# Kernel tuning notes

Hardware: AMD Instinct MI355X
Metric: run time of the kernel (lower is better)

The kernel has to match this reference:

```python
import jax, jax.numpy as jnp
import numpy as np

N, E, D, R = 50000, 625000, 128, 200
BN_EPS = 1e-5


def setup_inputs() -> dict:
    key = jax.random.key(0)
    ks = jax.random.split(key, 16)
    x = jax.random.normal(ks[0], (N, D), dtype=jnp.float32)
    r_feats = jax.random.normal(ks[1], (R, D), dtype=jnp.float32)
    src = jax.random.randint(ks[2], (E,), 0, N, dtype=jnp.int32)
    dst = jax.random.randint(ks[3], (E,), 0, N, dtype=jnp.int32)
    etype = jax.random.randint(ks[4], (E,), 0, R, dtype=jnp.int32)
    norm = jax.random.uniform(ks[5], (E, 1), dtype=jnp.float32)
    out_edges_mask = jax.random.randint(ks[6], (E,), 0, 2) == 1
    in_edges_mask = jnp.logical_not(out_edges_mask)  # masks partition edges
    s = 1.0 / np.sqrt(D)
    def lin(k):
        kw, kb = jax.random.split(k)
        return (jax.random.uniform(kw, (D, D), jnp.float32, -s, s),
                jax.random.uniform(kb, (D,), jnp.float32, -s, s))
    W_O_w, W_O_b = lin(ks[7])
    W_I_w, W_I_b = lin(ks[8])
    W_S_w, W_S_b = lin(ks[9])
    W_R_w, W_R_b = lin(ks[10])
    loop_rel = jax.random.normal(ks[11], (1, D), dtype=jnp.float32) * s  # xavier-ish
    bn_gamma = jnp.ones((D,), jnp.float32)
    bn_beta = jnp.zeros((D,), jnp.float32)
    return {"x": x, "r_feats": r_feats, "src": src, "dst": dst, "etype": etype,
            "norm": norm, "in_edges_mask": in_edges_mask, "out_edges_mask": out_edges_mask,
            "W_O_w": W_O_w, "W_O_b": W_O_b, "W_I_w": W_I_w, "W_I_b": W_I_b,
            "W_S_w": W_S_w, "W_S_b": W_S_b, "W_R_w": W_R_w, "W_R_b": W_R_b,
            "loop_rel": loop_rel, "bn_gamma": bn_gamma, "bn_beta": bn_beta}


def reference(x, r_feats, src, dst, etype, norm, in_edges_mask, out_edges_mask,
              W_O_w, W_O_b, W_I_w, W_I_b, W_S_w, W_S_b, W_R_w, W_R_b,
              loop_rel, bn_gamma, bn_beta):
    # r_feats with self-loop relation appended: [R+1, D]
    r_ext = jnp.concatenate([r_feats, loop_rel], axis=0)
    # per-edge relation feature scaled by norm: [E, D]
    e_h = r_ext[etype] * norm
    # compose (sub): u_sub_e -> src feature minus edge feature
    comp_h = x[src] - e_h
    # per-direction linear projections, selected by the edge partition masks
    h_O = comp_h @ W_O_w.T + W_O_b
    h_I = comp_h @ W_I_w.T + W_I_b
    new_comp_h = jnp.where(out_edges_mask[:, None], h_O, h_I)
    # scatter-sum messages to destination nodes: [N, D]
    agg = jax.ops.segment_sum(new_comp_h, dst, num_segments=x.shape[0])
    # self-loop branch (sub with loop relation)
    comp_h_s = x - r_ext[-1]
    n_out = (comp_h_s @ W_S_w.T + W_S_b + agg) * (1.0 / 3.0)  # dropout in eval mode
    # BatchNorm1d (training-mode batch stats, biased variance)
    mean = jnp.mean(n_out, axis=0)
    var = jnp.mean((n_out - mean) ** 2, axis=0)
    n_out = (n_out - mean) * jax.lax.rsqrt(var + BN_EPS) * bn_gamma + bn_beta
    n_out = jnp.tanh(n_out)
    r_out = r_ext @ W_R_w.T + W_R_b
    return n_out, r_out[:-1]
```

## Files before the change

### kernel.cpp

```cpp
#include <hip/hip_runtime.h>
#include <cstddef>

#define N_NODES 50000
#define N_EDGES 625000
#define DIM     128
#define R_REL   200
#define BN_EPS  1e-5f
#define SLOTS   64
#define ND4     ((N_NODES * DIM) / 4)
#define R4      ((R_REL * DIM) / 4)

typedef __bf16 bf16x8 __attribute__((ext_vector_type(8)));
typedef float  f32x4  __attribute__((ext_vector_type(4)));

__device__ __forceinline__ float bfu2f(unsigned int hi16) {
    return __uint_as_float(hi16);
}
__device__ __forceinline__ unsigned int f2bfr(float f) {
    unsigned int u = __float_as_uint(f);
    return (u + 0x7fffu + ((u >> 16) & 1u)) >> 16;
}

__global__ __launch_bounds__(256) void init_kernel(
    const float* __restrict__ x, ushort* __restrict__ xb,
    const float* __restrict__ rf, ushort* __restrict__ rb,
    int* __restrict__ cnt, float* __restrict__ colsum, float* __restrict__ colsq,
    const unsigned char* __restrict__ in_m, const unsigned char* __restrict__ out_m,
    int* __restrict__ flag) {
    int gid = blockIdx.x * 256 + threadIdx.x;
    int total = gridDim.x * 256;
    for (int i = gid; i < ND4; i += total) {
        float4 v = ((const float4*)x)[i];
        ushort4 o;
        o.x = (ushort)f2bfr(v.x); o.y = (ushort)f2bfr(v.y);
        o.z = (ushort)f2bfr(v.z); o.w = (ushort)f2bfr(v.w);
        ((ushort4*)xb)[i] = o;
    }
    if (gid < R4) {
        float4 v = ((const float4*)rf)[gid];
        ushort4 o;
        o.x = (ushort)f2bfr(v.x); o.y = (ushort)f2bfr(v.y);
        o.z = (ushort)f2bfr(v.z); o.w = (ushort)f2bfr(v.w);
        ((ushort4*)rb)[gid] = o;
    }
    for (int i = gid; i < N_NODES; i += total) cnt[i] = 0;
    if (gid < DIM) { colsum[gid] = 0.f; colsq[gid] = 0.f; }
    if (blockIdx.x == 0) {
        int ok = (((int)in_m[threadIdx.x] + (int)out_m[threadIdx.x]) == 1) ? 1 : 0;
        __shared__ int sred[4];
        unsigned long long b = __ballot(ok);
        if ((threadIdx.x & 63) == 0) sred[threadIdx.x >> 6] = (b == ~0ULL) ? 1 : 0;
        __syncthreads();
        if (threadIdx.x == 0) *flag = sred[0] & sred[1] & sred[2] & sred[3];
    }
}

__global__ __launch_bounds__(384) void prep_weights_kernel(
    const float* __restrict__ WO, const float* __restrict__ WI,
    const float* __restrict__ WS, const float* __restrict__ loop,
    const float* __restrict__ bS, const float* __restrict__ bO,
    const float* __restrict__ bI, ushort* __restrict__ Wb,
    float* __restrict__ bias0, float* __restrict__ bO3, float* __restrict__ bI3) {
    int f = blockIdx.x;
    int k = threadIdx.x;
    const float third = 1.0f / 3.0f;
    float w;
    if (k < 128)      w = WS[f * DIM + k];
    else if (k < 256) w = WO[f * DIM + (k - 128)];
    else              w = WI[f * DIM + (k - 256)];
    Wb[f * 384 + k] = (ushort)f2bfr(w * third);
    __shared__ float red[128];
    if (k < 128) red[k] = loop[k] * WS[f * DIM + k];
    __syncthreads();
    for (int off = 64; off; off >>= 1) {
        if (k < off) red[k] += red[k + off];
        __syncthreads();
    }
    if (k == 0)   bias0[f] = (bS[f] - red[0]) * third;
    if (k == 64)  bO3[f] = bO[f] * third;
    if (k == 128) bI3[f] = bI[f] * third;
}

__global__ __launch_bounds__(128) void rout_kernel(const float* __restrict__ rf,
                                                   const float* __restrict__ WR,
                                                   const float* __restrict__ bR,
                                                   float* __restrict__ out) {
    int r = blockIdx.x;
    int f = threadIdx.x;
    __shared__ float row[DIM];
    row[f] = rf[r * DIM + f];
    __syncthreads();
    float acc = bR[f];
    for (int k = 0; k < DIM; ++k) acc += row[k] * WR[f * DIM + k];
    out[r * DIM + f] = acc;
}

__global__ __launch_bounds__(256) void slot_fill_kernel(
    const int* __restrict__ dst, const int* __restrict__ src,
    const int* __restrict__ et, const float* __restrict__ norm,
    const void* __restrict__ omask, const int* __restrict__ flag,
    int* __restrict__ cnt, uint2* __restrict__ erec) {
    int e = blockIdx.x * 256 + threadIdx.x;
    if (e >= N_EDGES) return;
    int fl = *flag;
    bool m = fl ? (((const unsigned char*)omask)[e] != 0)
                : (((const int*)omask)[e] != 0);
    int d = dst[e];
    int k = atomicAdd(&cnt[d], 1);
    if (k < SLOTS) {
        unsigned w0 = (unsigned)src[e] | ((unsigned)et[e] << 16) | (m ? 0x80000000u : 0u);
        erec[(size_t)d * SLOTS + k] = make_uint2(w0, (unsigned)__float_as_int(norm[e]));
    }
}

#define AGG_CALC(EX, EY, XW, RW)                                   \
    {                                                              \
        float nm = __uint_as_float(EY);                            \
        float fm = (float)((EX) >> 31);                            \
        float x0 = bfu2f((XW) << 16), x1 = bfu2f((XW) & 0xffff0000u); \
        float r0 = bfu2f((RW) << 16), r1 = bfu2f((RW) & 0xffff0000u); \
        float v0 = __builtin_fmaf(-nm, r0, x0);                    \
        float v1 = __builtin_fmaf(-nm, r1, x1);                    \
        aT0 += v0; aT1 += v1;                                      \
        aO0 = __builtin_fmaf(fm, v0, aO0);                         \
        aO1 = __builtin_fmaf(fm, v1, aO1);                         \
        cOf += fm;                                                 \
    }

__global__ __launch_bounds__(256, 8) void aggregate_kernel(
    const unsigned int* __restrict__ xb,
    const unsigned int* __restrict__ rb,
    const uint2* __restrict__ erec,
    const int* __restrict__ cnt,
    unsigned int* __restrict__ S_Ob, unsigned int* __restrict__ S_Ib,
    float* __restrict__ cntO, float* __restrict__ cntI) {
    int wv = threadIdx.x >> 6;
    unsigned lane = threadIdx.x & 63;
    int n = blockIdx.x * 4 + wv;
    if (n >= N_NODES) return;
    int deg = cnt[n];
    deg = deg < SLOTS ? deg : SLOTS;
    int beg = n * SLOTS, end = beg + deg;

    float aT0 = 0.f, aT1 = 0.f, aO0 = 0.f, aO1 = 0.f, cOf = 0.f;

    int j = beg;
    for (; j + 7 < end; j += 8) {
        uint2 e0 = erec[j],     e1 = erec[j + 1], e2 = erec[j + 2], e3 = erec[j + 3];
        uint2 e4 = erec[j + 4], e5 = erec[j + 5], e6 = erec[j + 6], e7 = erec[j + 7];
        unsigned xw0 = xb[((e0.x & 0xffffu) << 6) + lane];
        unsigned rw0 = rb[(((e0.x >> 16) & 0x7fffu) << 6) + lane];
        unsigned xw1 = xb[((e1.x & 0xffffu) << 6) + lane];
        unsigned rw1 = rb[(((e1.x >> 16) & 0x7fffu) << 6) + lane];
        unsigned xw2 = xb[((e2.x & 0xffffu) << 6) + lane];
        unsigned rw2 = rb[(((e2.x >> 16) & 0x7fffu) << 6) + lane];
        unsigned xw3 = xb[((e3.x & 0xffffu) << 6) + lane];
        unsigned rw3 = rb[(((e3.x >> 16) & 0x7fffu) << 6) + lane];
        unsigned xw4 = xb[((e4.x & 0xffffu) << 6) + lane];
        unsigned rw4 = rb[(((e4.x >> 16) & 0x7fffu) << 6) + lane];
        unsigned xw5 = xb[((e5.x & 0xffffu) << 6) + lane];
        unsigned rw5 = rb[(((e5.x >> 16) & 0x7fffu) << 6) + lane];
        unsigned xw6 = xb[((e6.x & 0xffffu) << 6) + lane];
        unsigned rw6 = rb[(((e6.x >> 16) & 0x7fffu) << 6) + lane];
        unsigned xw7 = xb[((e7.x & 0xffffu) << 6) + lane];
        unsigned rw7 = rb[(((e7.x >> 16) & 0x7fffu) << 6) + lane];
        AGG_CALC(e0.x, e0.y, xw0, rw0)
        AGG_CALC(e1.x, e1.y, xw1, rw1)
        AGG_CALC(e2.x, e2.y, xw2, rw2)
        AGG_CALC(e3.x, e3.y, xw3, rw3)
        AGG_CALC(e4.x, e4.y, xw4, rw4)
        AGG_CALC(e5.x, e5.y, xw5, rw5)
        AGG_CALC(e6.x, e6.y, xw6, rw6)
        AGG_CALC(e7.x, e7.y, xw7, rw7)
    }
    for (; j < end; ++j) {
        uint2 e0 = erec[j];
        unsigned xw0 = xb[((e0.x & 0xffffu) << 6) + lane];
        unsigned rw0 = rb[(((e0.x >> 16) & 0x7fffu) << 6) + lane];
        AGG_CALC(e0.x, e0.y, xw0, rw0)
    }

    float aI0 = aT0 - aO0, aI1 = aT1 - aO1;
    S_Ob[((unsigned)n << 6) + lane] = f2bfr(aO0) | (f2bfr(aO1) << 16);
    S_Ib[((unsigned)n << 6) + lane] = f2bfr(aI0) | (f2bfr(aI1) << 16);
    if (lane == 0) { cntO[n] = cOf; cntI[n] = (float)deg - cOf; }
}

__global__ __launch_bounds__(256, 4) void gemm_kernel(
    const ushort* __restrict__ xb, const ushort* __restrict__ S_Ob,
    const ushort* __restrict__ S_Ib, const ushort* __restrict__ Wb,
    const float* __restrict__ bias0, const float* __restrict__ bO3,
    const float* __restrict__ bI3, const float* __restrict__ cntO,
    const float* __restrict__ cntI, float* __restrict__ y,
    float* __restrict__ colsum, float* __restrict__ colsq) {
    __shared__ ushort Bs[128][136];
    __shared__ float redS[4][128];
    __shared__ float redQ[4][128];

    int tid = threadIdx.x;
    int wv = tid >> 6, lane = tid & 63;
    int cl = lane & 15, kg = lane >> 4;
    int wrow0 = blockIdx.x * 64 + wv * 16;

    f32x4 acc[8];
#pragma unroll
    for (int cf = 0; cf < 8; ++cf) acc[cf] = (f32x4){0.f, 0.f, 0.f, 0.f};

    int rowA = wrow0 + cl;
    int rowc = rowA < N_NODES ? rowA : N_NODES - 1;
    const ushort* Abase[3] = {xb, S_Ob, S_Ib};

    for (int kq = 0; kq < 3; ++kq) {
        __syncthreads();
#pragma unroll
        for (int j = 0; j < 8; ++j) {
            int i = tid + j * 256;
            int col = i >> 4, k8 = (i & 15) << 3;
            uint4 w = *(const uint4*)(Wb + (size_t)col * 384 + kq * 128 + k8);
            *(uint4*)&Bs[col][k8] = w;
        }
        const ushort* Ap0 = Abase[kq] + (size_t)rowc * 128 + kg * 8;
        uint4 a4[4];
#pragma unroll
        for (int ks = 0; ks < 4; ++ks) a4[ks] = *(const uint4*)(Ap0 + ks * 32);
        __syncthreads();
#pragma unroll
        for (int ks = 0; ks < 4; ++ks) {
            bf16x8 af = __builtin_bit_cast(bf16x8, a4[ks]);
#pragma unroll
            for (int cf = 0; cf < 8; ++cf) {
                bf16x8 bv = __builtin_bit_cast(bf16x8,
                    *(const uint4*)&Bs[cf * 16 + cl][ks * 32 + kg * 8]);
                acc[cf] = __builtin_amdgcn_mfma_f32_16x16x32_bf16(af, bv, acc[cf], 0, 0, 0);
            }
        }
    }

    float b0a[8], boa[8], bia[8];
#pragma unroll
    for (int cf = 0; cf < 8; ++cf) {
        int col = cf * 16 + cl;
        b0a[cf] = bias0[col]; boa[cf] = bO3[col]; bia[cf] = bI3[col];
    }
    float cOv[4], cIv[4]; int rows[4]; bool rv[4];
#pragma unroll
    for (int r = 0; r < 4; ++r) {
        int row = wrow0 + kg * 4 + r;
        rows[r] = row; rv[r] = row < N_NODES;
        cOv[r] = rv[r] ? cntO[row] : 0.f;
        cIv[r] = rv[r] ? cntI[row] : 0.f;
    }
    float ps[8], pq[8];
#pragma unroll
    for (int cf = 0; cf < 8; ++cf) {
        float s = 0.f, q = 0.f;
        int col = cf * 16 + cl;
#pragma unroll
        for (int r = 0; r < 4; ++r) {
            if (rv[r]) {
                float v = acc[cf][r] + b0a[cf] + cOv[r] * boa[cf] + cIv[r] * bia[cf];
                y[(size_t)rows[r] * DIM + col] = v;
                s += v; q += v * v;
            }
        }
        s += __shfl_xor(s, 16);
        s += __shfl_xor(s, 32);
        q += __shfl_xor(q, 16);
        q += __shfl_xor(q, 32);
        ps[cf] = s; pq[cf] = q;
    }
    if (kg == 0) {
#pragma unroll
        for (int cf = 0; cf < 8; ++cf) {
            redS[wv][cf * 16 + cl] = ps[cf];
            redQ[wv][cf * 16 + cl] = pq[cf];
        }
    }
    __syncthreads();
    if (tid < 128) {
        float s = redS[0][tid] + redS[1][tid] + redS[2][tid] + redS[3][tid];
        float q = redQ[0][tid] + redQ[1][tid] + redQ[2][tid] + redQ[3][tid];
        atomicAdd(colsum + tid, s);
        atomicAdd(colsq + tid, q);
    }
}

__global__ __launch_bounds__(256) void bn_apply_kernel(
    float* __restrict__ y, const float* __restrict__ colsum, const float* __restrict__ colsq,
    const float* __restrict__ gamma, const float* __restrict__ beta) {
    __shared__ __align__(16) float sc[DIM];
    __shared__ __align__(16) float sh[DIM];
    int tid = threadIdx.x;
    if (tid < DIM) {
        float mean = colsum[tid] * (1.0f / N_NODES);
        float var  = colsq[tid] * (1.0f / N_NODES) - mean * mean;
        float s = rsqrtf(var + BN_EPS) * gamma[tid];
        sc[tid] = s;
        sh[tid] = beta[tid] - mean * s;
    }
    __syncthreads();
    const int total4 = N_NODES * 32;
    for (int i = blockIdx.x * 256 + tid; i < total4; i += gridDim.x * 256) {
        float4 s4 = ((const float4*)sc)[i & 31];
        float4 h4 = ((const float4*)sh)[i & 31];
        float4 v = ((float4*)y)[i];
        v.x = tanhf(v.x * s4.x + h4.x);
        v.y = tanhf(v.y * s4.y + h4.y);
        v.z = tanhf(v.z * s4.z + h4.z);
        v.w = tanhf(v.w * s4.w + h4.w);
        ((float4*)y)[i] = v;
    }
}

extern "C" void kernel_launch(void* const* d_in, const int* in_sizes, int n_in,
                              void* d_out, int out_size, void* d_ws, size_t ws_size,
                              hipStream_t stream) {
    const float* x        = (const float*)d_in[0];
    const float* r_feats  = (const float*)d_in[1];
    const int*   src      = (const int*)d_in[2];
    const int*   dst      = (const int*)d_in[3];
    const int*   etype    = (const int*)d_in[4];
    const float* norm     = (const float*)d_in[5];
    const void*  in_mask  = d_in[6];
    const void*  out_mask = d_in[7];
    const float* W_O_w    = (const float*)d_in[8];
    const float* W_O_b    = (const float*)d_in[9];
    const float* W_I_w    = (const float*)d_in[10];
    const float* W_I_b    = (const float*)d_in[11];
    const float* W_S_w    = (const float*)d_in[12];
    const float* W_S_b    = (const float*)d_in[13];
    const float* W_R_w    = (const float*)d_in[14];
    const float* W_R_b    = (const float*)d_in[15];
    const float* loop_rel = (const float*)d_in[16];
    const float* bn_gamma = (const float*)d_in[17];
    const float* bn_beta  = (const float*)d_in[18];

    const size_t ND = (size_t)N_NODES * DIM;
    char* p = (char*)d_ws;
    auto alloc = [&](size_t bytes) { void* r = (void*)p; p += (bytes + 255) & ~(size_t)255; return r; };

    ushort* S_Ob = (ushort*)alloc(ND * 2);
    ushort* S_Ib = (ushort*)alloc(ND * 2);
    ushort* xb   = (ushort*)alloc(ND * 2);
    ushort* rb   = (ushort*)alloc((size_t)R_REL * DIM * 2);
    uint2* erec  = (uint2*)alloc((size_t)N_NODES * SLOTS * 8);
    ushort* Wb   = (ushort*)alloc((size_t)DIM * 384 * 2);
    float* bias0 = (float*)alloc(DIM * 4);
    float* bO3   = (float*)alloc(DIM * 4);
    float* bI3   = (float*)alloc(DIM * 4);
    float* colsum= (float*)alloc(DIM * 4);
    float* colsq = (float*)alloc(DIM * 4);
    float* cntO  = (float*)alloc(N_NODES * 4);
    float* cntI  = (float*)alloc(N_NODES * 4);
    int*   cnt   = (int*)alloc(N_NODES * 4);
    int*   flag  = (int*)alloc(4);

    float* y    = (float*)d_out;
    float* rout = (float*)d_out + ND;

    init_kernel<<<6250, 256, 0, stream>>>(
        x, xb, r_feats, rb, cnt, colsum, colsq,
        (const unsigned char*)in_mask, (const unsigned char*)out_mask, flag);

    prep_weights_kernel<<<128, 384, 0, stream>>>(
        W_O_w, W_I_w, W_S_w, loop_rel, W_S_b, W_O_b, W_I_b,
        Wb, bias0, bO3, bI3);

    rout_kernel<<<R_REL, 128, 0, stream>>>(r_feats, W_R_w, W_R_b, rout);

    slot_fill_kernel<<<(N_EDGES + 255) / 256, 256, 0, stream>>>(
        dst, src, etype, norm, out_mask, flag, cnt, erec);

    aggregate_kernel<<<(N_NODES + 3) / 4, 256, 0, stream>>>(
        (const unsigned int*)xb, (const unsigned int*)rb, erec, cnt,
        (unsigned int*)S_Ob, (unsigned int*)S_Ib, cntO, cntI);

    gemm_kernel<<<(N_NODES + 63) / 64, 256, 0, stream>>>(
        xb, S_Ob, S_Ib, Wb, bias0, bO3, bI3, cntO, cntI, y, colsum, colsq);

    bn_apply_kernel<<<2048, 256, 0, stream>>>(y, colsum, colsq, bn_gamma, bn_beta);
}
```

Before: 136.5 us.

## Fuse edge slot-fill, bf16 conversion, weight prep and r_out into one launch

Merges the edge slot-fill, x/r bf16 conversion, weight/bias preparation and relation projection into a single kernel that dispatches on block index ranges. A tiny init kernel now only zeroes counts and sets the mask-format flag. The aim is to cut launch overhead and let the independent front-end stages run concurrently instead of serialising. The trade-off is a heterogeneous kernel whose register and occupancy budget is set by its heaviest branch. Early returns in the fill branch are safe because those blocks never reach a barrier.

Result: no change. 136.4 us (-0.1%).

```diff
diff --git a/kernel.cpp b/kernel.cpp
--- a/kernel.cpp
+++ b/kernel.cpp
@@ -10,6 +10,14 @@
 #define ND4     ((N_NODES * DIM) / 4)
 #define R4      ((R_REL * DIM) / 4)
 
+#define NB_FILL  2442
+#define NB_CONV  3200
+#define PREP_BASE (NB_FILL + NB_CONV)
+#define NB_PREP  128
+#define ROUT_BASE (PREP_BASE + NB_PREP)
+#define NB_ROUT  100
+#define NB_TOTAL (ROUT_BASE + NB_ROUT)
+
 typedef __bf16 bf16x8 __attribute__((ext_vector_type(8)));
 typedef float  f32x4  __attribute__((ext_vector_type(4)));
 
@@ -21,30 +29,12 @@
     return (u + 0x7fffu + ((u >> 16) & 1u)) >> 16;
 }
 
-__global__ __launch_bounds__(256) void init_kernel(
-    const float* __restrict__ x, ushort* __restrict__ xb,
-    const float* __restrict__ rf, ushort* __restrict__ rb,
-    int* __restrict__ cnt, float* __restrict__ colsum, float* __restrict__ colsq,
+__global__ __launch_bounds__(256) void init0_kernel(
+    int* __restrict__ cnt,
     const unsigned char* __restrict__ in_m, const unsigned char* __restrict__ out_m,
     int* __restrict__ flag) {
     int gid = blockIdx.x * 256 + threadIdx.x;
-    int total = gridDim.x * 256;
-    for (int i = gid; i < ND4; i += total) {
-        float4 v = ((const float4*)x)[i];
-        ushort4 o;
-        o.x = (ushort)f2bfr(v.x); o.y = (ushort)f2bfr(v.y);
-        o.z = (ushort)f2bfr(v.z); o.w = (ushort)f2bfr(v.w);
-        ((ushort4*)xb)[i] = o;
-    }
-    if (gid < R4) {
-        float4 v = ((const float4*)rf)[gid];
-        ushort4 o;
-        o.x = (ushort)f2bfr(v.x); o.y = (ushort)f2bfr(v.y);
-        o.z = (ushort)f2bfr(v.z); o.w = (ushort)f2bfr(v.w);
-        ((ushort4*)rb)[gid] = o;
-    }
-    for (int i = gid; i < N_NODES; i += total) cnt[i] = 0;
-    if (gid < DIM) { colsum[gid] = 0.f; colsq[gid] = 0.f; }
+    if (gid < N_NODES) cnt[gid] = 0;
     if (blockIdx.x == 0) {
         int ok = (((int)in_m[threadIdx.x] + (int)out_m[threadIdx.x]) == 1) ? 1 : 0;
         __shared__ int sred[4];
@@ -55,61 +45,81 @@
     }
 }
 
-__global__ __launch_bounds__(384) void prep_weights_kernel(
+__global__ __launch_bounds__(256) void fused_front_kernel(
+    const int* __restrict__ dst, const int* __restrict__ src,
+    const int* __restrict__ et, const float* __restrict__ norm,
+    const void* __restrict__ omask, const int* __restrict__ flag,
+    int* __restrict__ cnt, uint2* __restrict__ erec,
+    const float* __restrict__ x, ushort* __restrict__ xb,
+    const float* __restrict__ rf, ushort* __restrict__ rb,
     const float* __restrict__ WO, const float* __restrict__ WI,
     const float* __restrict__ WS, const float* __restrict__ loop,
     const float* __restrict__ bS, const float* __restrict__ bO,
     const float* __restrict__ bI, ushort* __restrict__ Wb,
-    float* __restrict__ bias0, float* __restrict__ bO3, float* __restrict__ bI3) {
-    int f = blockIdx.x;
-    int k = threadIdx.x;
-    const float third = 1.0f / 3.0f;
-    float w;
-    if (k < 128)      w = WS[f * DIM + k];
-    else if (k < 256) w = WO[f * DIM + (k - 128)];
-    else              w = WI[f * DIM + (k - 256)];
-    Wb[f * 384 + k] = (ushort)f2bfr(w * third);
-    __shared__ float red[128];
-    if (k < 128) red[k] = loop[k] * WS[f * DIM + k];
-    __syncthreads();
-    for (int off = 64; off; off >>= 1) {
-        if (k < off) red[k] += red[k + off];
-        __syncthreads();
-    }
-    if (k == 0)   bias0[f] = (bS[f] - red[0]) * third;
-    if (k == 64)  bO3[f] = bO[f] * third;
-    if (k == 128) bI3[f] = bI[f] * third;
-}
-
-__global__ __launch_bounds__(128) void rout_kernel(const float* __restrict__ rf,
-                                                   const float* __restrict__ WR,
-                                                   const float* __restrict__ bR,
-                                                   float* __restrict__ out) {
-    int r = blockIdx.x;
-    int f = threadIdx.x;
-    __shared__ float row[DIM];
-    row[f] = rf[r * DIM + f];
-    __syncthreads();
-    float acc = bR[f];
-    for (int k = 0; k < DIM; ++k) acc += row[k] * WR[f * DIM + k];
-    out[r * DIM + f] = acc;
-}
-
-__global__ __launch_bounds__(256) void slot_fill_kernel(
-    const int* __restrict__ dst, const int* __restrict__ src,
-    const int* __restrict__ et, const float* __restrict__ norm,
-    const void* __restrict__ omask, const int* __restrict__ flag,
-    int* __restrict__ cnt, uint2* __restrict__ erec) {
-    int e = blockIdx.x * 256 + threadIdx.x;
-    if (e >= N_EDGES) return;
-    int fl = *flag;
-    bool m = fl ? (((const unsigned char*)omask)[e] != 0)
-                : (((const int*)omask)[e] != 0);
-    int d = dst[e];
-    int k = atomicAdd(&cnt[d], 1);
-    if (k < SLOTS) {
-        unsigned w0 = (unsigned)src[e] | ((unsigned)et[e] << 16) | (m ? 0x80000000u : 0u);
-        erec[(size_t)d * SLOTS + k] = make_uint2(w0, (unsigned)__float_as_int(norm[e]));
+    float* __restrict__ bias0, float* __restrict__ bO3, float* __restrict__ bI3,
+    float* __restrict__ colsum, float* __restrict__ colsq,
+    const float* __restrict__ WR, const float* __restrict__ bR,
+    float* __restrict__ rout) {
+    __shared__ float smem[256];
+    int b = blockIdx.x, t = threadIdx.x;
+
+    if (b < NB_FILL) {
+        int e = b * 256 + t;
+        if (e >= N_EDGES) return;
+        int fl = *flag;
+        bool m = fl ? (((const unsigned char*)omask)[e] != 0)
+                    : (((const int*)omask)[e] != 0);
+        int d = dst[e];
+        int k = atomicAdd(&cnt[d], 1);
+        if (k < SLOTS) {
+            unsigned w0 = (unsigned)src[e] | ((unsigned)et[e] << 16) | (m ? 0x80000000u : 0u);
+            erec[(size_t)d * SLOTS + k] = make_uint2(w0, (unsigned)__float_as_int(norm[e]));
+        }
+    } else if (b < PREP_BASE) {
+        int cgid = (b - NB_FILL) * 256 + t;
+        for (int i = cgid; i < ND4; i += NB_CONV * 256) {
+            float4 v = ((const float4*)x)[i];
+            ushort4 o;
+            o.x = (ushort)f2bfr(v.x); o.y = (ushort)f2bfr(v.y);
+            o.z = (ushort)f2bfr(v.z); o.w = (ushort)f2bfr(v.w);
+            ((ushort4*)xb)[i] = o;
+        }
+        if (cgid < R4) {
+            float4 v = ((const float4*)rf)[cgid];
+            ushort4 o;
+            o.x = (ushort)f2bfr(v.x); o.y = (ushort)f2bfr(v.y);
+            o.z = (ushort)f2bfr(v.z); o.w = (ushort)f2bfr(v.w);
+            ((ushort4*)rb)[cgid] = o;
+        }
+    } else if (b < ROUT_BASE) {
+        int f = b - PREP_BASE;
+        const float third = 1.0f / 3.0f;
+        for (int k = t; k < 384; k += 256) {
+            float w;
+            if (k < 128)      w = WS[f * DIM + k];
+            else if (k < 256) w = WO[f * DIM + (k - 128)];
+            else              w = WI[f * DIM + (k - 256)];
+            Wb[f * 384 + k] = (ushort)f2bfr(w * third);
+        }
+        if (t < 128) smem[t] = loop[t] * WS[f * DIM + t];
+        __syncthreads();
+        for (int off = 64; off; off >>= 1) {
+            if (t < off) smem[t] += smem[t + off];
+            __syncthreads();
+        }
+        if (t == 0) bias0[f] = (bS[f] - smem[0]) * third;
+        if (t == 1) bO3[f] = bO[f] * third;
+        if (t == 2) bI3[f] = bI[f] * third;
+        if (f == 0 && t >= 128) { colsum[t - 128] = 0.f; colsq[t - 128] = 0.f; }
+    } else {
+        float* row2 = smem;
+        int rloc = t >> 7, f = t & 127;
+        int r = (b - ROUT_BASE) * 2 + rloc;
+        row2[rloc * 128 + f] = rf[r * DIM + f];
+        __syncthreads();
+        float acc = bR[f];
+        for (int k = 0; k < DIM; ++k) acc += row2[rloc * 128 + k] * WR[f * DIM + k];
+        rout[r * DIM + f] = acc;
     }
 }
 
@@ -358,18 +368,15 @@
     float* y    = (float*)d_out;
     float* rout = (float*)d_out + ND;
 
-    init_kernel<<<6250, 256, 0, stream>>>(
-        x, xb, r_feats, rb, cnt, colsum, colsq,
-        (const unsigned char*)in_mask, (const unsigned char*)out_mask, flag);
-
-    prep_weights_kernel<<<128, 384, 0, stream>>>(
+    init0_kernel<<<(N_NODES + 255) / 256, 256, 0, stream>>>(
+        cnt, (const unsigned char*)in_mask, (const unsigned char*)out_mask, flag);
+
+    fused_front_kernel<<<NB_TOTAL, 256, 0, stream>>>(
+        dst, src, etype, norm, out_mask, flag, cnt, erec,
+        x, xb, r_feats, rb,
         W_O_w, W_I_w, W_S_w, loop_rel, W_S_b, W_O_b, W_I_b,
-        Wb, bias0, bO3, bI3);
-
-    rout_kernel<<<R_REL, 128, 0, stream>>>(r_feats, W_R_w, W_R_b, rout);
-
-    slot_fill_kernel<<<(N_EDGES + 255) / 256, 256, 0, stream>>>(
-        dst, src, etype, norm, out_mask, flag, cnt, erec);
+        Wb, bias0, bO3, bI3, colsum, colsq,
+        W_R_w, W_R_b, rout);
 
     aggregate_kernel<<<(N_NODES + 3) / 4, 256, 0, stream>>>(
         (const unsigned int*)xb, (const unsigned int*)rb, erec, cnt,
```
